# Kernel tuning notes

Measured on AMD Instinct MI355X. Metric: run time of the kernel, lower is better.

## Reference

```python
import jax, jax.numpy as jnp
import numpy as np


def setup_inputs() -> dict:
    key = jax.random.key(0)
    k1, k2 = jax.random.split(key)
    N, D = 8192, 64
    mag = jax.random.uniform(k1, (N, D), dtype=jnp.float32)
    phase = jax.random.normal(k2, (N, D), dtype=jnp.float32)
    return {"mag": mag, "phase": phase}


def reference(mag, phase):
    # score_ij = sum_d mag_i,d * mag_j,d * cos(phase_i,d - phase_j,d)
    # expanded via cos(a-b) = cos a cos b + sin a sin b into two GEMMs,
    # mathematically identical to the O(N^2 D) broadcasted form.
    a = mag * jnp.cos(phase)  # [N, D]
    b = mag * jnp.sin(phase)  # [N, D]
    scores = a @ a.T + b @ b.T  # [N, N]
    attn = jax.nn.softmax(scores, axis=1)
    new_mag = attn @ mag      # [N, D]
    new_phase = attn @ phase  # [N, D]
    return new_mag, new_phase
```

## Files before the change

kernel.cpp:

```cpp
#include <hip/hip_runtime.h>
#include <hip/hip_bf16.h>

typedef __attribute__((ext_vector_type(8))) short short8;
typedef __attribute__((ext_vector_type(4))) float f32x4;
typedef __attribute__((ext_vector_type(16))) float f32x16;
typedef __attribute__((ext_vector_type(2))) int int2v;

#define N_TOK 8192
#define D_HALF 64
#define D_FULL 128
#define QB 128
#define KQ 2048
#define CHUNK 128
#define NCH (KQ / CHUNK)
#define OSTR 132
#define THR 8.0f

__global__ __launch_bounds__(256) void precompute_kernel(
    const float* __restrict__ mag, const float* __restrict__ phase,
    __hip_bfloat16* __restrict__ Kf, __hip_bfloat16* __restrict__ Vf)
{
    int idx = blockIdx.x * 256 + threadIdx.x;
    if (idx >= N_TOK * D_HALF) return;
    int n = idx >> 6, d0 = idx & 63;
    float m = mag[idx], p = phase[idx];
    float s, c;
    sincosf(p, &s, &c);
    {
        float val[2] = { m * c, m * s };
        #pragma unroll
        for (int h = 0; h < 2; ++h) {
            int dc = d0 + 64 * h;
            int off = ((n >> 5) * 16 + (dc >> 4) * 2 + ((dc >> 3) & 1)) * 256
                      + (n & 31) * 8 + (dc & 7);
            Kf[off] = __float2bfloat16(val[h]);
        }
    }
    {
        float val[2] = { m, p };
        #pragma unroll
        for (int h = 0; h < 2; ++h) {
            int dv = d0 + 64 * h;
            int off = ((n >> 4) * 4 + (dv >> 5)) * 512 + ((n >> 3) & 1) * 256
                      + (dv & 31) * 8 + (n & 7);
            Vf[off] = __float2bfloat16(val[h]);
        }
    }
}

static __device__ __forceinline__ unsigned bfpair(float lo, float hi)
{
    __hip_bfloat16 l = __float2bfloat16(lo), h = __float2bfloat16(hi);
    unsigned short ul = *reinterpret_cast<unsigned short*>(&l);
    unsigned short uh = *reinterpret_cast<unsigned short*>(&h);
    return (unsigned)ul | ((unsigned)uh << 16);
}

__global__ __launch_bounds__(512, 2) void attn_kernel(
    const short8* __restrict__ Kf8, const short8* __restrict__ Vf8,
    float* __restrict__ Opart, float* __restrict__ Mp, float* __restrict__ Sp)
{
    __shared__ __align__(16) char smem[131072];

    const int tid  = threadIdx.x;
    const int wid  = tid >> 6;
    const int lane = tid & 63;
    const int li   = lane & 31;
    const int hi   = lane >> 5;
    const int qh   = wid >> 1;
    const int kp   = wid & 1;

    const int bid  = blockIdx.x;
    const int qt   = bid >> 2;
    const int kq   = bid & 3;
    const int rot  = bid & (NCH - 1);

    float (*O_lds)[32][OSTR] = (float (*)[32][OSTR])smem;
    float* ms_base = (float*)(smem + 67584);
    auto msm = [&](int slot, int which) -> float* { return ms_base + (slot * 2 + which) * 32; };

    auto stageKV = [&](int ck, char* lbase) {
        const char* gk = (const char*)(Kf8 + (size_t)ck * 2048);
        const char* gv = (const char*)(Vf8 + (size_t)ck * 2048);
        #pragma unroll
        for (int j = 0; j < 4; ++j)
            __builtin_amdgcn_global_load_lds(
                (const __attribute__((address_space(1))) void*)(gk + j * 8192 + tid * 16),
                (__attribute__((address_space(3))) void*)(lbase + j * 8192 + tid * 16),
                16, 0, 0);
        #pragma unroll
        for (int j = 0; j < 4; ++j)
            __builtin_amdgcn_global_load_lds(
                (const __attribute__((address_space(1))) void*)(gv + j * 8192 + tid * 16),
                (__attribute__((address_space(3))) void*)(lbase + 32768 + j * 8192 + tid * 16),
                16, 0, 0);
    };
    auto ck_of = [&](int t) { return kq * NCH + ((t + rot) & (NCH - 1)); };

    short8 bq[8];
    {
        const short8* qp = Kf8 + (size_t)(qt * 4 + qh) * 512;
        #pragma unroll
        for (int ks = 0; ks < 8; ++ks)
            bq[ks] = qp[(ks * 2 + hi) * 32 + li];
    }

    f32x16 acc[4];
    #pragma unroll
    for (int d = 0; d < 4; ++d) acc[d] = (f32x16)(0.0f);
    float mrow = -3.0e38f, srow = 0.0f;

    stageKV(ck_of(0), smem);
    stageKV(ck_of(1), smem + 65536);
    asm volatile("s_waitcnt vmcnt(8)");
    __builtin_amdgcn_s_barrier();

    for (int t = 0; t < NCH; ++t) {
        char* base = smem + (t & 1) * 65536;
        const short8* ldsK = (const short8*)base;
        const short8* ldsV = (const short8*)(base + 32768);

        #pragma unroll
        for (int pp = 0; pp < 2; ++pp) {
            const int panel = kp + 2 * pp;

            f32x16 st = (f32x16)(0.0f);
            __builtin_amdgcn_s_setprio(1);
            #pragma unroll
            for (int ks = 0; ks < 8; ++ks) {
                short8 kf = ldsK[panel * 512 + (ks * 2 + hi) * 32 + li];
                st = __builtin_amdgcn_mfma_f32_32x32x16_bf16(kf, bq[ks], st, 0, 0, 0);
            }
            __builtin_amdgcn_s_setprio(0);

            float mx[8];
            #pragma unroll
            for (int r = 0; r < 8; ++r) mx[r] = fmaxf(st[r], st[r + 8]);
            #pragma unroll
            for (int w = 4; w >= 1; w >>= 1)
                #pragma unroll
                for (int r = 0; r < w; ++r) mx[r] = fmaxf(mx[r], mx[r + w]);
            float pmax = fmaxf(mx[0], __shfl_xor(mx[0], 32));

            if (!__all(pmax - mrow <= THR)) {
                float mn  = fmaxf(mrow, pmax);
                float scl = __expf(mrow - mn);
                srow *= scl;
                #pragma unroll
                for (int d = 0; d < 4; ++d)
                    #pragma unroll
                    for (int r = 0; r < 16; ++r) acc[d][r] *= scl;
                mrow = mn;
            }

            #pragma unroll
            for (int r = 0; r < 16; ++r) st[r] = __expf(st[r] - mrow);
            float sm[8];
            #pragma unroll
            for (int r = 0; r < 8; ++r) sm[r] = st[r] + st[r + 8];
            #pragma unroll
            for (int w = 4; w >= 1; w >>= 1)
                #pragma unroll
                for (int r = 0; r < w; ++r) sm[r] += sm[r + w];
            srow += sm[0] + __shfl_xor(sm[0], 32);

            #pragma unroll
            for (int c = 0; c < 2; ++c) {
                const int b = 8 * c;
                unsigned a0 = bfpair(st[b + 0], st[b + 1]);
                unsigned a1 = bfpair(st[b + 2], st[b + 3]);
                unsigned b0 = bfpair(st[b + 4], st[b + 5]);
                unsigned b1 = bfpair(st[b + 6], st[b + 7]);
                int2v r0 = __builtin_amdgcn_permlane32_swap((int)a0, (int)b0, false, false);
                int2v r1 = __builtin_amdgcn_permlane32_swap((int)a1, (int)b1, false, false);
                union { int w[4]; short8 v; } u;
                u.w[0] = r0[0]; u.w[1] = r1[0]; u.w[2] = r0[1]; u.w[3] = r1[1];

                const short8* vp = ldsV + (panel * 2 + c) * 256 + hi * 32 + li;
                __builtin_amdgcn_s_setprio(1);
                #pragma unroll
                for (int d = 0; d < 4; ++d) {
                    short8 vf = vp[d * 64];
                    acc[d] = __builtin_amdgcn_mfma_f32_32x32x16_bf16(vf, u.v, acc[d], 0, 0, 0);
                }
                __builtin_amdgcn_s_setprio(0);
            }
        }

        __builtin_amdgcn_s_barrier();
        if (t + 2 < NCH) {
            stageKV(ck_of(t + 2), base);
            asm volatile("s_waitcnt vmcnt(8)");
        } else {
            asm volatile("s_waitcnt vmcnt(0)");
        }
        __builtin_amdgcn_s_barrier();
    }

    auto store_partial = [&](int slot) {
        #pragma unroll
        for (int d = 0; d < 4; ++d)
            #pragma unroll
            for (int rr = 0; rr < 4; ++rr) {
                f32x4 v;
                #pragma unroll
                for (int j = 0; j < 4; ++j) v[j] = acc[d][4 * rr + j];
                *reinterpret_cast<f32x4*>(&O_lds[slot][li][d * 32 + 8 * rr + 4 * hi]) = v;
            }
        if (hi == 0) { msm(slot, 0)[li] = mrow; msm(slot, 1)[li] = srow; }
    };
    auto merge_partial = [&](int slot) {
        float mb = msm(slot, 0)[li], sb = msm(slot, 1)[li];
        float M  = fmaxf(mrow, mb);
        float ea = __expf(mrow - M), eb = __expf(mb - M);
        srow = srow * ea + sb * eb;
        mrow = M;
        #pragma unroll
        for (int d = 0; d < 4; ++d)
            #pragma unroll
            for (int rr = 0; rr < 4; ++rr) {
                f32x4 v = *reinterpret_cast<const f32x4*>(&O_lds[slot][li][d * 32 + 8 * rr + 4 * hi]);
                #pragma unroll
                for (int j = 0; j < 4; ++j)
                    acc[d][4 * rr + j] = acc[d][4 * rr + j] * ea + v[j] * eb;
            }
    };

    __syncthreads();
    if (kp == 1) store_partial(qh);
    __syncthreads();
    if (kp == 0) merge_partial(qh);
    __syncthreads();
    if (kp == 0) store_partial(qh);
    __syncthreads();

    #pragma unroll
    for (int u0 = 0; u0 < 4; ++u0) {
        int u  = tid + u0 * 512;
        int q  = u >> 4;
        int dg = (u & 15) * 8;
        int grp = q >> 5, qq = q & 31;
        f32x4 o0 = *reinterpret_cast<const f32x4*>(&O_lds[grp][qq][dg]);
        f32x4 o1 = *reinterpret_cast<const f32x4*>(&O_lds[grp][qq][dg + 4]);
        size_t pidx = (size_t)bid * QB + q;
        *reinterpret_cast<f32x4*>(&Opart[pidx * D_FULL + dg])     = o0;
        *reinterpret_cast<f32x4*>(&Opart[pidx * D_FULL + dg + 4]) = o1;
        if (dg == 0) { Mp[pidx] = msm(grp, 0)[qq]; Sp[pidx] = msm(grp, 1)[qq]; }
    }
}

__global__ __launch_bounds__(256) void merge4_kernel(
    const float* __restrict__ Opart, const float* __restrict__ Mp,
    const float* __restrict__ Sp, float* __restrict__ out)
{
    int i   = blockIdx.x * 256 + threadIdx.x;
    int row = i >> 5;
    int dg  = (i & 31) * 4;
    int qt  = row >> 7, qq = row & 127;
    size_t pidx[4];
    float m[4], s[4];
    #pragma unroll
    for (int k = 0; k < 4; ++k) {
        pidx[k] = (size_t)(qt * 4 + k) * QB + qq;
        m[k] = Mp[pidx[k]];
        s[k] = Sp[pidx[k]];
    }
    float M = fmaxf(fmaxf(m[0], m[1]), fmaxf(m[2], m[3]));
    float e[4], S = 0.0f;
    #pragma unroll
    for (int k = 0; k < 4; ++k) { e[k] = __expf(m[k] - M); S += s[k] * e[k]; }
    float inv = 1.0f / S;
    f32x4 o = (f32x4)(0.0f);
    #pragma unroll
    for (int k = 0; k < 4; ++k) {
        f32x4 a = *reinterpret_cast<const f32x4*>(&Opart[pidx[k] * D_FULL + dg]);
        #pragma unroll
        for (int j = 0; j < 4; ++j) o[j] += a[j] * e[k];
    }
    #pragma unroll
    for (int j = 0; j < 4; ++j) o[j] *= inv;
    float* dst = (dg < D_HALF)
        ? out + (size_t)row * D_HALF + dg
        : out + (size_t)N_TOK * D_HALF + (size_t)row * D_HALF + (dg - D_HALF);
    *reinterpret_cast<f32x4*>(dst) = o;
}

extern "C" void kernel_launch(void* const* d_in, const int* in_sizes, int n_in,
                              void* d_out, int out_size, void* d_ws, size_t ws_size,
                              hipStream_t stream)
{
    const float* mag   = (const float*)d_in[0];
    const float* phase = (const float*)d_in[1];
    float* out = (float*)d_out;

    char* ws = (char*)d_ws;
    __hip_bfloat16* Kf = (__hip_bfloat16*)ws;
    __hip_bfloat16* Vf = Kf + (size_t)N_TOK * D_FULL;
    float* Opart = (float*)(ws + 4u * 1024 * 1024);
    float* Mp    = (float*)(ws + 20u * 1024 * 1024);
    float* Sp    = Mp + 32768;

    precompute_kernel<<<(N_TOK * D_HALF + 255) / 256, 256, 0, stream>>>(mag, phase, Kf, Vf);
    attn_kernel<<<256, 512, 0, stream>>>((const short8*)Kf, (const short8*)Vf, Opart, Mp, Sp);
    merge4_kernel<<<1024, 256, 0, stream>>>(Opart, Mp, Sp, out);
}
```

Before: 64.92 us.

## Fold log2e into K features, use exp2, and issue both QK panels first

```diff
diff --git a/kernel.cpp b/kernel.cpp
--- a/kernel.cpp
+++ b/kernel.cpp
@@ -15,6 +15,7 @@
 #define NCH (KQ / CHUNK)
 #define OSTR 132
 #define THR 8.0f
+#define RSC 1.2011224087864498f
 
 __global__ __launch_bounds__(256) void precompute_kernel(
     const float* __restrict__ mag, const float* __restrict__ phase,
@@ -27,7 +28,7 @@
     float s, c;
     sincosf(p, &s, &c);
     {
-        float val[2] = { m * c, m * s };
+        float val[2] = { m * c * RSC, m * s * RSC };
         #pragma unroll
         for (int h = 0; h < 2; ++h) {
             int dc = d0 + 64 * h;
@@ -110,6 +111,60 @@
     for (int d = 0; d < 4; ++d) acc[d] = (f32x16)(0.0f);
     float mrow = -3.0e38f, srow = 0.0f;
 
+    auto softmax = [&](f32x16& st) {
+        float mx[8];
+        #pragma unroll
+        for (int r = 0; r < 8; ++r) mx[r] = fmaxf(st[r], st[r + 8]);
+        float ma = fmaxf(fmaxf(mx[0], mx[1]), mx[2]);
+        float mb = fmaxf(fmaxf(mx[3], mx[4]), mx[5]);
+        float mc = fmaxf(mx[6], mx[7]);
+        float mm = fmaxf(fmaxf(ma, mb), mc);
+        float pmax = fmaxf(mm, __shfl_xor(mm, 32));
+        if (!__all(pmax - mrow <= THR)) {
+            float mn  = fmaxf(mrow, pmax);
+            float scl = exp2f(mrow - mn);
+            srow *= scl;
+            #pragma unroll
+            for (int d = 0; d < 4; ++d)
+                #pragma unroll
+                for (int r = 0; r < 16; ++r) acc[d][r] *= scl;
+            mrow = mn;
+        }
+        #pragma unroll
+        for (int r = 0; r < 16; ++r) st[r] = exp2f(st[r] - mrow);
+        float sm[8];
+        #pragma unroll
+        for (int r = 0; r < 8; ++r) sm[r] = st[r] + st[r + 8];
+        float sa = (sm[0] + sm[1]) + (sm[2] + sm[3]);
+        float sb = (sm[4] + sm[5]) + (sm[6] + sm[7]);
+        float ss = sa + sb;
+        srow += ss + __shfl_xor(ss, 32);
+    };
+
+    auto pv = [&](const f32x16& st, int panel, const short8* ldsV) {
+        #pragma unroll
+        for (int c = 0; c < 2; ++c) {
+            const int b = 8 * c;
+            unsigned a0 = bfpair(st[b + 0], st[b + 1]);
+            unsigned a1 = bfpair(st[b + 2], st[b + 3]);
+            unsigned b0 = bfpair(st[b + 4], st[b + 5]);
+            unsigned b1 = bfpair(st[b + 6], st[b + 7]);
+            int2v r0 = __builtin_amdgcn_permlane32_swap((int)a0, (int)b0, false, false);
+            int2v r1 = __builtin_amdgcn_permlane32_swap((int)a1, (int)b1, false, false);
+            union { int w[4]; short8 v; } u;
+            u.w[0] = r0[0]; u.w[1] = r1[0]; u.w[2] = r0[1]; u.w[3] = r1[1];
+
+            const short8* vp = ldsV + (panel * 2 + c) * 256 + hi * 32 + li;
+            __builtin_amdgcn_s_setprio(1);
+            #pragma unroll
+            for (int d = 0; d < 4; ++d) {
+                short8 vf = vp[d * 64];
+                acc[d] = __builtin_amdgcn_mfma_f32_32x32x16_bf16(vf, u.v, acc[d], 0, 0, 0);
+            }
+            __builtin_amdgcn_s_setprio(0);
+        }
+    };
+
     stageKV(ck_of(0), smem);
     stageKV(ck_of(1), smem + 65536);
     asm volatile("s_waitcnt vmcnt(8)");
@@ -119,73 +174,26 @@
         char* base = smem + (t & 1) * 65536;
         const short8* ldsK = (const short8*)base;
         const short8* ldsV = (const short8*)(base + 32768);
-
-        #pragma unroll
-        for (int pp = 0; pp < 2; ++pp) {
-            const int panel = kp + 2 * pp;
-
-            f32x16 st = (f32x16)(0.0f);
-            __builtin_amdgcn_s_setprio(1);
-            #pragma unroll
-            for (int ks = 0; ks < 8; ++ks) {
-                short8 kf = ldsK[panel * 512 + (ks * 2 + hi) * 32 + li];
-                st = __builtin_amdgcn_mfma_f32_32x32x16_bf16(kf, bq[ks], st, 0, 0, 0);
-            }
-            __builtin_amdgcn_s_setprio(0);
-
-            float mx[8];
-            #pragma unroll
-            for (int r = 0; r < 8; ++r) mx[r] = fmaxf(st[r], st[r + 8]);
-            #pragma unroll
-            for (int w = 4; w >= 1; w >>= 1)
-                #pragma unroll
-                for (int r = 0; r < w; ++r) mx[r] = fmaxf(mx[r], mx[r + w]);
-            float pmax = fmaxf(mx[0], __shfl_xor(mx[0], 32));
-
-            if (!__all(pmax - mrow <= THR)) {
-                float mn  = fmaxf(mrow, pmax);
-                float scl = __expf(mrow - mn);
-                srow *= scl;
-                #pragma unroll
-                for (int d = 0; d < 4; ++d)
-                    #pragma unroll
-                    for (int r = 0; r < 16; ++r) acc[d][r] *= scl;
-                mrow = mn;
-            }
-
-            #pragma unroll
-            for (int r = 0; r < 16; ++r) st[r] = __expf(st[r] - mrow);
-            float sm[8];
-            #pragma unroll
-            for (int r = 0; r < 8; ++r) sm[r] = st[r] + st[r + 8];
-            #pragma unroll
-            for (int w = 4; w >= 1; w >>= 1)
-                #pragma unroll
-                for (int r = 0; r < w; ++r) sm[r] += sm[r + w];
-            srow += sm[0] + __shfl_xor(sm[0], 32);
-
-            #pragma unroll
-            for (int c = 0; c < 2; ++c) {
-                const int b = 8 * c;
-                unsigned a0 = bfpair(st[b + 0], st[b + 1]);
-                unsigned a1 = bfpair(st[b + 2], st[b + 3]);
-                unsigned b0 = bfpair(st[b + 4], st[b + 5]);
-                unsigned b1 = bfpair(st[b + 6], st[b + 7]);
-                int2v r0 = __builtin_amdgcn_permlane32_swap((int)a0, (int)b0, false, false);
-                int2v r1 = __builtin_amdgcn_permlane32_swap((int)a1, (int)b1, false, false);
-                union { int w[4]; short8 v; } u;
-                u.w[0] = r0[0]; u.w[1] = r1[0]; u.w[2] = r0[1]; u.w[3] = r1[1];
-
-                const short8* vp = ldsV + (panel * 2 + c) * 256 + hi * 32 + li;
-                __builtin_amdgcn_s_setprio(1);
-                #pragma unroll
-                for (int d = 0; d < 4; ++d) {
-                    short8 vf = vp[d * 64];
-                    acc[d] = __builtin_amdgcn_mfma_f32_32x32x16_bf16(vf, u.v, acc[d], 0, 0, 0);
-                }
-                __builtin_amdgcn_s_setprio(0);
-            }
-        }
+        const int p0 = kp, p1 = kp + 2;
+
+        f32x16 st0 = (f32x16)(0.0f), st1 = (f32x16)(0.0f);
+        __builtin_amdgcn_s_setprio(1);
+        #pragma unroll
+        for (int ks = 0; ks < 8; ++ks) {
+            short8 kf = ldsK[p0 * 512 + (ks * 2 + hi) * 32 + li];
+            st0 = __builtin_amdgcn_mfma_f32_32x32x16_bf16(kf, bq[ks], st0, 0, 0, 0);
+        }
+        #pragma unroll
+        for (int ks = 0; ks < 8; ++ks) {
+            short8 kf = ldsK[p1 * 512 + (ks * 2 + hi) * 32 + li];
+            st1 = __builtin_amdgcn_mfma_f32_32x32x16_bf16(kf, bq[ks], st1, 0, 0, 0);
+        }
+        __builtin_amdgcn_s_setprio(0);
+
+        softmax(st0);
+        pv(st0, p0, ldsV);
+        softmax(st1);
+        pv(st1, p1, ldsV);
 
         __builtin_amdgcn_s_barrier();
         if (t + 2 < NCH) {
@@ -212,7 +220,7 @@
     auto merge_partial = [&](int slot) {
         float mb = msm(slot, 0)[li], sb = msm(slot, 1)[li];
         float M  = fmaxf(mrow, mb);
-        float ea = __expf(mrow - M), eb = __expf(mb - M);
+        float ea = exp2f(mrow - M), eb = exp2f(mb - M);
         srow = srow * ea + sb * eb;
         mrow = M;
         #pragma unroll
@@ -268,7 +276,7 @@
     float M = fmaxf(fmaxf(m[0], m[1]), fmaxf(m[2], m[3]));
     float e[4], S = 0.0f;
     #pragma unroll
-    for (int k = 0; k < 4; ++k) { e[k] = __expf(m[k] - M); S += s[k] * e[k]; }
+    for (int k = 0; k < 4; ++k) { e[k] = exp2f(m[k] - M); S += s[k] * e[k]; }
     float inv = 1.0f / S;
     f32x4 o = (f32x4)(0.0f);
     #pragma unroll
```

New measurement: 73.31 us. 12.9% more time.
